# Performance work log

Hardware: AMD Instinct MI355X
Metric: run time of the kernel (lower is better)

Reference implementation:

```python
import jax, jax.numpy as jnp
import numpy as np

ANCHORS = np.array([[10,13],[16,30],[33,23],[30,61],[62,45],[59,119],[116,90],[156,198],[373,326]], dtype=np.float32)
ANCHOR_MASK = [[6,7,8],[3,4,5],[0,1,2]]
CLASS_NUM = 80
IGNORE_THRESH = 0.5


def _bce_mean(z, x):
    # Keras BinaryCrossentropy(from_logits=True) called as a loss object:
    # elementwise sigmoid-CE, mean over last axis, then SUM_OVER_BATCH_SIZE
    # reduction == mean over ALL elements -> scalar.
    ce = jnp.maximum(x, 0.0) - x * z + jnp.log1p(jnp.exp(-jnp.abs(x)))
    return jnp.mean(ce)


def _layer_loss(out, lab, anchors):
    B, gh, gw, _ = out.shape
    A = anchors.shape[0]
    feats = out.reshape(B, gh, gw, A, CLASS_NUM + 5)
    anchors = jnp.asarray(anchors, dtype=jnp.float32)  # [A,2] (w,h)
    inp_wh = jnp.array([gw * 32, gh * 32], dtype=jnp.float32)  # reverse(input_shape)
    grid_wh = jnp.array([gw, gh], dtype=jnp.float32)           # reverse(grid_shape)

    gy, gx = jnp.meshgrid(jnp.arange(gh), jnp.arange(gw), indexing='ij')
    grid = jnp.stack([gx, gy], axis=-1).astype(jnp.float32)[:, :, None, :]  # [gh,gw,1,2]

    pred_xy = (jax.nn.sigmoid(feats[..., 0:2]) + grid) / grid_wh
    pred_wh = jnp.exp(feats[..., 2:4]) * anchors / inp_wh
    pred_box = jnp.concatenate([pred_xy, pred_wh], axis=-1)  # [B,gh,gw,A,4]

    obj = lab[..., 4:5]          # [B,gh,gw,A,1]
    objb = obj != 0.0
    N = gh * gw * A

    def _per_image(args):
        pb, tb, valid = args  # pb: [N,4] predicted, tb: [N,4] label boxes, valid: [N] bool
        b1_xy, b1_wh = pb[:, None, 0:2], pb[:, None, 2:4]
        b2_xy, b2_wh = tb[None, :, 0:2], tb[None, :, 2:4]
        b1_mins, b1_maxes = b1_xy - b1_wh / 2.0, b1_xy + b1_wh / 2.0
        b2_mins, b2_maxes = b2_xy - b2_wh / 2.0, b2_xy + b2_wh / 2.0
        inter_mins = jnp.maximum(b1_mins, b2_mins)
        inter_maxes = jnp.maximum(b1_maxes, b2_maxes)  # faithful to source (uses maximum, not minimum)
        inter_wh = jnp.maximum(inter_maxes - inter_mins, 0.0)
        inter = inter_wh[..., 0] * inter_wh[..., 1]
        a1 = b1_wh[..., 0] * b1_wh[..., 1]
        a2 = b2_wh[..., 0] * b2_wh[..., 1]
        iou = inter / (a1 + a2 - inter)  # [N,N]
        # only true boxes count; empty set -> best=-1 (matches tf reduce_max of empty = -inf)
        iou = jnp.where(valid[None, :], iou, -1.0)
        best_iou = jnp.max(iou, axis=-1)
        return (best_iou < IGNORE_THRESH).astype(jnp.float32)

    ignore = jax.lax.map(_per_image, (pred_box.reshape(B, N, 4),
                                      lab[..., 0:4].reshape(B, N, 4),
                                      objb.reshape(B, N)))
    ignore = jax.lax.stop_gradient(ignore).reshape(B, gh, gw, A, 1)

    raw_true_xy = lab[..., 0:2] * grid_wh - grid
    raw_true_wh = jnp.log(lab[..., 2:4] * inp_wh / anchors)
    raw_true_wh = jnp.where(objb, raw_true_wh, 0.0)
    box_loss_scale = 2.0 - lab[..., 2:3] * lab[..., 3:4]

    bf = jnp.float32(B)
    xy_loss = jnp.sum(obj * box_loss_scale * _bce_mean(raw_true_xy, feats[..., 0:2])) / bf
    wh_loss = jnp.sum(obj * box_loss_scale * 0.5 * jnp.square(raw_true_wh - feats[..., 2:4])) / bf
    conf_bce = _bce_mean(obj, feats[..., 4:5])
    conf_loss = jnp.sum(obj * conf_bce + (1.0 - obj) * conf_bce * ignore) / bf
    class_loss = jnp.sum(obj * _bce_mean(lab[..., 5:], feats[..., 5:])) / bf
    return xy_loss + wh_loss + conf_loss + class_loss


def _make_labels(key, B, g):
    k1, k2, k3, k4 = jax.random.split(key, 4)
    xy = jax.random.uniform(k1, (B, g, g, 3, 2), dtype=jnp.float32)
    wh = jax.random.uniform(k2, (B, g, g, 3, 2), dtype=jnp.float32, minval=0.05, maxval=1.0)
    objness = (jax.random.uniform(k3, (B, g, g, 3, 1)) < 0.02).astype(jnp.float32)
    cls = (jax.random.uniform(k4, (B, g, g, 3, CLASS_NUM)) < 0.05).astype(jnp.float32)
    return jnp.concatenate([xy, wh, objness, cls], axis=-1)


def setup_inputs() -> dict:
    key = jax.random.key(0)
    ks = jax.random.split(key, 6)
    B = 8
    grids = [13, 26, 52]
    out = {}
    for i, g in enumerate(grids):
        out[f'o{i}'] = jax.random.normal(ks[i], (B, g, g, 3 * (CLASS_NUM + 5)), dtype=jnp.float32)
        out[f'l{i}'] = _make_labels(ks[3 + i], B, g)
    return out


def reference(o0, o1, o2, l0, l1, l2):
    outputs = (o0, o1, o2)
    labels = (l0, l1, l2)
    loss = jnp.float32(0.0)
    for l in range(3):
        loss = loss + _layer_loss(outputs[l], labels[l], ANCHORS[ANCHOR_MASK[l]])
    return loss
```

## Files before the change

### kernel.cpp

```cpp
#include <hip/hip_runtime.h>
#include <math.h>

#define BDIM 256
#define NSTREAMB 1769
#define NCELLB 334
#define NBLK_A (NSTREAMB + NCELLB)
#define NB_IGNORE 336
#define SCAP 1024

__device__ __constant__ float c_aw[3][3] = {{116.f,156.f,373.f},{30.f,62.f,59.f},{10.f,16.f,33.f}};
__device__ __constant__ float c_ah[3][3] = {{90.f,198.f,326.f},{61.f,45.f,119.f},{13.f,30.f,23.f}};


__device__ __forceinline__ float bce_fast(float z, float x) {
    float t = __expf(-fabsf(x));
    return fmaxf(x, 0.f) - x * z + __logf(1.f + t);
}
__device__ __forceinline__ float bce4(const float4& z, const float4& x) {
    return bce_fast(z.x, x.x) + bce_fast(z.y, x.y)
         + bce_fast(z.z, x.z) + bce_fast(z.w, x.w);
}

__global__ __launch_bounds__(BDIM) void mega_a(
    const float* __restrict__ o0, const float* __restrict__ l0,
    const float* __restrict__ o1, const float* __restrict__ l1,
    const float* __restrict__ o2, const float* __restrict__ l2,
    double* __restrict__ accq7, int* __restrict__ done,
    double* __restrict__ slotS, double* __restrict__ slotC,
    float4* __restrict__ pbox, float* __restrict__ noobj)
{
    if (blockIdx.x < NSTREAMB) {
        if (blockIdx.x == 0 && threadIdx.x == 0) {
            accq7[0] = 0.0; accq7[1] = 0.0; accq7[2] = 0.0; *done = 0;
        }
        int blk0, n4;
        const float4 *O4, *L4;
        if (blockIdx.x < 85)       { blk0=0;   n4=86190;   O4=(const float4*)o0; L4=(const float4*)l0; }
        else if (blockIdx.x < 422) { blk0=85;  n4=344760;  O4=(const float4*)o1; L4=(const float4*)l1; }
        else                       { blk0=422; n4=1379040; O4=(const float4*)o2; L4=(const float4*)l2; }

        int rb   = (int)blockIdx.x - blk0;
        int base = rb * (BDIM * 4) + (int)threadIdx.x;
        float s0 = 0.f, s1 = 0.f, s2 = 0.f, s3 = 0.f;
        if ((rb + 1) * (BDIM * 4) <= n4) {
            float4 a0 = O4[base];          float4 b0 = L4[base];
            float4 a1 = O4[base +   BDIM]; float4 b1 = L4[base +   BDIM];
            float4 a2 = O4[base + 2*BDIM]; float4 b2 = L4[base + 2*BDIM];
            float4 a3 = O4[base + 3*BDIM]; float4 b3 = L4[base + 3*BDIM];
            s0 = bce4(b0, a0); s1 = bce4(b1, a1);
            s2 = bce4(b2, a2); s3 = bce4(b3, a3);
        } else {
            #pragma unroll
            for (int k = 0; k < 4; k++) {
                int j = base + k * BDIM;
                if (j < n4) { float4 a = O4[j], b = L4[j]; s0 += bce4(b, a); }
            }
        }
        float s = (s0 + s1) + (s2 + s3);
        __shared__ float sb[4];
        #pragma unroll
        for (int off = 32; off > 0; off >>= 1) s += __shfl_down(s, off, 64);
        if ((threadIdx.x & 63) == 0) sb[threadIdx.x >> 6] = s;
        __syncthreads();
        if (threadIdx.x == 0)
            slotS[blockIdx.x] = (double)sb[0] + (double)sb[1]
                              + (double)sb[2] + (double)sb[3];
        return;
    }

    int cb = blockIdx.x - NSTREAMB;
    int layer, cblk0;
    if (cb < 16)      { layer = 0; cblk0 = 0; }
    else if (cb < 80) { layer = 1; cblk0 = 16; }
    else              { layer = 2; cblk0 = 80; }
    const int g     = (layer == 0) ? 13 : (layer == 1) ? 26 : 52;
    const int Nlimg = g * g * 3;
    const int Cl    = 8 * Nlimg;
    const int cbase = (layer == 0) ? 0 : (layer == 1) ? 4056 : 20280;
    const float* O  = (layer == 0) ? o0 : (layer == 1) ? o1 : o2;
    const float* L  = (layer == 0) ? l0 : (layer == 1) ? l1 : l2;
    const float gf  = (float)g;
    const float inp = gf * 32.f;

    int  cell = (cb - cblk0) * BDIM + (int)threadIdx.x;
    bool live = (cell < Cl);
    float s_sub=0.f, s_xy=0.f, s_wh=0.f, s_conf=0.f, s_obj=0.f, s_s1=0.f;
    if (live) {
        const float* op = O + (size_t)cell * 85;
        const float* lp = L + (size_t)cell * 85;
        float x0=op[0], x1=op[1], x2=op[2], x3=op[3], x4=op[4];
        float lx=lp[0], ly=lp[1], lw=lp[2], lh=lp[3], lobj=lp[4];
        int a  = cell % 3;
        int xi = (cell / 3) % g;
        int yi = (cell / (3 * g)) % g;
        float aw = c_aw[layer][a], ah = c_ah[layer][a];

        float c4 = bce_fast(lobj, x4);
        s_sub  = bce_fast(lx,x0) + bce_fast(ly,x1)
               + bce_fast(lw,x2) + bce_fast(lh,x3) + c4;
        s_conf = c4;
        s_obj  = lobj;
        s_xy   = bce_fast(lx*gf - (float)xi, x0) + bce_fast(ly*gf - (float)yi, x1);

        float px = (1.f/(1.f+expf(-x0)) + (float)xi) / gf;
        float py = (1.f/(1.f+expf(-x1)) + (float)yi) / gf;
        float pw = expf(x2) * aw / inp;
        float ph = expf(x3) * ah / inp;
        pbox[cbase + cell]  = make_float4(px, py, pw, ph);
        noobj[cbase + cell] = 1.f - lobj;

        if (lobj != 0.f) {
            float bls = 2.f - lw * lh;
            s_s1 = lobj * bls;
            float dw = logf(lw * inp / aw) - x2;
            float dh = logf(lh * inp / ah) - x3;
            s_wh = lobj * bls * 0.5f * (dw * dw + dh * dh);
        }
    }

    __shared__ float sb6[6][4];
    float v[6] = {s_sub, s_xy, s_wh, s_conf, s_obj, s_s1};
    #pragma unroll
    for (int q = 0; q < 6; q++) {
        float x = v[q];
        #pragma unroll
        for (int off = 32; off > 0; off >>= 1) x += __shfl_down(x, off, 64);
        if ((threadIdx.x & 63) == 0) sb6[q][threadIdx.x >> 6] = x;
    }
    __syncthreads();
    if (threadIdx.x < 6) {
        int q = threadIdx.x;
        slotC[cb * 6 + q] = (double)sb6[q][0] + (double)sb6[q][1]
                          + (double)sb6[q][2] + (double)sb6[q][3];
    }
}

__global__ __launch_bounds__(BDIM) void ignore_fin(
    const float* __restrict__ l0, const float* __restrict__ l1,
    const float* __restrict__ l2,
    double* __restrict__ accq7, int* __restrict__ done,
    const double* __restrict__ slotS, const double* __restrict__ slotC,
    const float4* __restrict__ pbox, const float* __restrict__ noobj,
    float* __restrict__ out)
{
    int layer, img, chunk;
    if (blockIdx.x < 16)      { layer = 0; img = blockIdx.x >> 1; chunk = blockIdx.x & 1; }
    else if (blockIdx.x < 80) { int t = blockIdx.x - 16; layer = 1; img = t >> 3; chunk = t & 7; }
    else                      { int t = blockIdx.x - 80; layer = 2; img = t >> 5; chunk = t & 31; }
    const int g     = (layer == 0) ? 13 : (layer == 1) ? 26 : 52;
    const int Nlimg = g * g * 3;
    const int cbase = (layer == 0) ? 0 : (layer == 1) ? 4056 : 20280;
    const float* L  = (layer == 0) ? l0 : (layer == 1) ? l1 : l2;

    int ci = chunk * BDIM + (int)threadIdx.x;
    bool live = (ci < Nlimg);
    int cell = cbase + img * Nlimg + (live ? ci : 0);

    float pminx=0, pmaxx=0, pminy=0, pmaxy=0, a1=0, nb=0;
    if (live) {
        float4 p = pbox[cell];
        pminx = p.x - p.z*0.5f; pmaxx = p.x + p.z*0.5f;
        pminy = p.y - p.w*0.5f; pmaxy = p.y + p.w*0.5f;
        a1 = p.z * p.w;
        nb = noobj[cell];
    }

    __shared__ int    sIdx[SCAP];
    __shared__ int    sN;
    __shared__ float4 sT[SCAP];
    if (threadIdx.x == 0) sN = 0;
    __syncthreads();
    const float* nob = noobj + cbase + img * Nlimg;
    for (int i = threadIdx.x; i < Nlimg; i += BDIM) {
        if (nob[i] == 0.0f) {
            int p = atomicAdd(&sN, 1);
            if (p < SCAP) sIdx[p] = i;
        }
    }
    __syncthreads();
    int n = min(sN, SCAP);
    for (int i = threadIdx.x; i < n; i += BDIM) {
        const float* lp = L + (size_t)(img * Nlimg + sIdx[i]) * 85;
        sT[i] = make_float4(lp[0], lp[1], lp[2], lp[3]);
    }
    __syncthreads();

    float best = -1.f;
    if (live) {
        for (int j = 0; j < n; j++) {
            float4 t = sT[j];
            float hw = t.z*0.5f, hh = t.w*0.5f;
            float imnx = fmaxf(pminx, t.x - hw);
            float imxx = fmaxf(pmaxx, t.x + hw);
            float imny = fmaxf(pminy, t.y - hh);
            float imxy = fmaxf(pmaxy, t.y + hh);
            float iw = fmaxf(imxx - imnx, 0.f);
            float ih = fmaxf(imxy - imny, 0.f);
            float inter = iw * ih;
            float iou = inter / (a1 + t.z*t.w - inter);
            best = fmaxf(best, iou);
            if (best >= 0.5f) break;
        }
    }

    float v = (live && best < 0.5f) ? nb : 0.f;
    __shared__ float sbr[4];
    #pragma unroll
    for (int off = 32; off > 0; off >>= 1) v += __shfl_down(v, off, 64);
    if ((threadIdx.x & 63) == 0) sbr[threadIdx.x >> 6] = v;
    __syncthreads();
    __shared__ int isLast;
    if (threadIdx.x == 0) {
        double t = (double)sbr[0] + (double)sbr[1] + (double)sbr[2] + (double)sbr[3];
        atomicAdd(&accq7[layer], t);
        __threadfence();
        int old = atomicAdd(done, 1);
        isLast = (old == NB_IGNORE - 1) ? 1 : 0;
    }
    __syncthreads();
    if (!isLast) return;

    __threadfence();
    double qs0=0, qs1=0, qs2=0;
    for (int i = threadIdx.x; i < NSTREAMB; i += BDIM) {
        double x = slotS[i];
        if (i < 85) qs0 += x; else if (i < 422) qs1 += x; else qs2 += x;
    }
    double c00=0,c01=0,c02=0,c03=0,c04=0,c05=0;
    double c10=0,c11=0,c12=0,c13=0,c14=0,c15=0;
    double c20=0,c21=0,c22=0,c23=0,c24=0,c25=0;
#define CSUM(LO, HI, A0,A1,A2,A3,A4,A5)                                      \
    for (int i = (LO)*6 + (int)threadIdx.x; i < (HI)*6; i += BDIM) {         \
        int q = i % 6; double x = slotC[i];                                  \
        if      (q == 0) A0 += x; else if (q == 1) A1 += x;                  \
        else if (q == 2) A2 += x; else if (q == 3) A3 += x;                  \
        else if (q == 4) A4 += x; else             A5 += x;                  \
    }
    CSUM(0,   16,  c00,c01,c02,c03,c04,c05)
    CSUM(16,  80,  c10,c11,c12,c13,c14,c15)
    CSUM(80,  334, c20,c21,c22,c23,c24,c25)

    __shared__ double dsum[21][4];
    {
        double vals[21] = {qs0,qs1,qs2,
                           c00,c01,c02,c03,c04,c05,
                           c10,c11,c12,c13,c14,c15,
                           c20,c21,c22,c23,c24,c25};
        int lane = threadIdx.x & 63, wid = threadIdx.x >> 6;
        #pragma unroll
        for (int k = 0; k < 21; k++) {
            double r = vals[k];
            #pragma unroll
            for (int off = 32; off > 0; off >>= 1) r += __shfl_down(r, off, 64);
            if (lane == 0) dsum[k][wid] = r;
        }
    }
    __syncthreads();
    if (threadIdx.x == 0) {
        double loss = 0.0;
        const int gsz[3] = {13, 26, 52};
        for (int l = 0; l < 3; l++) {
            double C = 8.0 * gsz[l] * gsz[l] * 3.0;
            double Q0 = dsum[l][0] + dsum[l][1] + dsum[l][2] + dsum[l][3];
            double Qs[6];
            for (int j = 0; j < 6; j++) {
                int k = 3 + l * 6 + j;
                Qs[j] = dsum[k][0] + dsum[k][1] + dsum[k][2] + dsum[k][3];
            }
            double q7 = __hip_atomic_load(&accq7[l], __ATOMIC_RELAXED,
                                          __HIP_MEMORY_SCOPE_AGENT);
            double cls = (Q0 - Qs[0]) / (C * 80.0);
            loss += ( (Qs[1]/(C*2.0))*Qs[5] + Qs[2]
                    + (Qs[3]/C)*(Qs[4]+q7) + cls*Qs[4] ) / 8.0;
        }
        out[0] = (float)loss;
    }
}

extern "C" void kernel_launch(void* const* d_in, const int* in_sizes, int n_in,
                              void* d_out, int out_size, void* d_ws, size_t ws_size,
                              hipStream_t stream)
{
    const float* o0 = (const float*)d_in[0];
    const float* l0 = (const float*)d_in[1];
    const float* o1 = (const float*)d_in[2];
    const float* l1 = (const float*)d_in[3];
    const float* o2 = (const float*)d_in[4];
    const float* l2 = (const float*)d_in[5];

    double* accq7 = (double*)d_ws;
    int*    done  = (int*)((char*)d_ws + 24);
    double* slotS = (double*)((char*)d_ws + 64);
    double* slotC = (double*)((char*)d_ws + 14336);
    float4* pbox  = (float4*)((char*)d_ws + 30720);
    float*  noobj = (float*)((char*)d_ws + 1393664);

    mega_a<<<NBLK_A, BDIM, 0, stream>>>(o0, l0, o1, l1, o2, l2,
                                        accq7, done, slotS, slotC, pbox, noobj);
    ignore_fin<<<NB_IGNORE, BDIM, 0, stream>>>(l0, l1, l2,
                                               accq7, done, slotS, slotC,
                                               pbox, noobj, (float*)d_out);
}
```

Measured before the change: 151.9 us.

## Replace atomic last-block finalization with separate finalize kernel; schedule cell blocks first

Drops the atomic accumulation and done-counter last-block pattern from the ignore kernel. Per-block partials now go to a slot array, and a separate single-block kernel reduces them. The mega kernel also reorders its blocks so the cell-processing blocks, which produce pbox and noobj, get dispatched before the streaming BCE blocks. The aim is to remove atomics and fences and finish the dependency-critical work earlier, at the cost of one extra kernel launch.

```diff
diff --git a/kernel.cpp b/kernel.cpp
--- a/kernel.cpp
+++ b/kernel.cpp
@@ -2,9 +2,9 @@
 #include <math.h>
 
 #define BDIM 256
+#define NCELLB 334
 #define NSTREAMB 1769
-#define NCELLB 334
-#define NBLK_A (NSTREAMB + NCELLB)
+#define NBLK_A (NCELLB + NSTREAMB)
 #define NB_IGNORE 336
 #define SCAP 1024
 
@@ -25,21 +25,18 @@
     const float* __restrict__ o0, const float* __restrict__ l0,
     const float* __restrict__ o1, const float* __restrict__ l1,
     const float* __restrict__ o2, const float* __restrict__ l2,
-    double* __restrict__ accq7, int* __restrict__ done,
     double* __restrict__ slotS, double* __restrict__ slotC,
     float4* __restrict__ pbox, float* __restrict__ noobj)
 {
-    if (blockIdx.x < NSTREAMB) {
-        if (blockIdx.x == 0 && threadIdx.x == 0) {
-            accq7[0] = 0.0; accq7[1] = 0.0; accq7[2] = 0.0; *done = 0;
-        }
+    if (blockIdx.x >= NCELLB) {
+        int sb = blockIdx.x - NCELLB;
         int blk0, n4;
         const float4 *O4, *L4;
-        if (blockIdx.x < 85)       { blk0=0;   n4=86190;   O4=(const float4*)o0; L4=(const float4*)l0; }
-        else if (blockIdx.x < 422) { blk0=85;  n4=344760;  O4=(const float4*)o1; L4=(const float4*)l1; }
-        else                       { blk0=422; n4=1379040; O4=(const float4*)o2; L4=(const float4*)l2; }
-
-        int rb   = (int)blockIdx.x - blk0;
+        if (sb < 85)       { blk0=0;   n4=86190;   O4=(const float4*)o0; L4=(const float4*)l0; }
+        else if (sb < 422) { blk0=85;  n4=344760;  O4=(const float4*)o1; L4=(const float4*)l1; }
+        else               { blk0=422; n4=1379040; O4=(const float4*)o2; L4=(const float4*)l2; }
+
+        int rb   = sb - blk0;
         int base = rb * (BDIM * 4) + (int)threadIdx.x;
         float s0 = 0.f, s1 = 0.f, s2 = 0.f, s3 = 0.f;
         if ((rb + 1) * (BDIM * 4) <= n4) {
@@ -57,18 +54,18 @@
             }
         }
         float s = (s0 + s1) + (s2 + s3);
-        __shared__ float sb[4];
+        __shared__ float sb4[4];
         #pragma unroll
         for (int off = 32; off > 0; off >>= 1) s += __shfl_down(s, off, 64);
-        if ((threadIdx.x & 63) == 0) sb[threadIdx.x >> 6] = s;
+        if ((threadIdx.x & 63) == 0) sb4[threadIdx.x >> 6] = s;
         __syncthreads();
         if (threadIdx.x == 0)
-            slotS[blockIdx.x] = (double)sb[0] + (double)sb[1]
-                              + (double)sb[2] + (double)sb[3];
+            slotS[sb] = (double)sb4[0] + (double)sb4[1]
+                      + (double)sb4[2] + (double)sb4[3];
         return;
     }
 
-    int cb = blockIdx.x - NSTREAMB;
+    int cb = blockIdx.x;
     int layer, cblk0;
     if (cb < 16)      { layer = 0; cblk0 = 0; }
     else if (cb < 80) { layer = 1; cblk0 = 16; }
@@ -100,7 +97,8 @@
                + bce_fast(lw,x2) + bce_fast(lh,x3) + c4;
         s_conf = c4;
         s_obj  = lobj;
-        s_xy   = bce_fast(lx*gf - (float)xi, x0) + bce_fast(ly*gf - (float)yi, x1);
+        s_xy   = bce_fast(lx*gf - (float)xi, x0)
+               + bce_fast(ly*gf - (float)yi, x1);
 
         float px = (1.f/(1.f+expf(-x0)) + (float)xi) / gf;
         float py = (1.f/(1.f+expf(-x1)) + (float)yi) / gf;
@@ -135,13 +133,11 @@
     }
 }
 
-__global__ __launch_bounds__(BDIM) void ignore_fin(
+__global__ __launch_bounds__(BDIM) void ignore_nb(
     const float* __restrict__ l0, const float* __restrict__ l1,
     const float* __restrict__ l2,
-    double* __restrict__ accq7, int* __restrict__ done,
-    const double* __restrict__ slotS, const double* __restrict__ slotC,
     const float4* __restrict__ pbox, const float* __restrict__ noobj,
-    float* __restrict__ out)
+    double* __restrict__ slotB)
 {
     int layer, img, chunk;
     if (blockIdx.x < 16)      { layer = 0; img = blockIdx.x >> 1; chunk = blockIdx.x & 1; }
@@ -209,46 +205,42 @@
     for (int off = 32; off > 0; off >>= 1) v += __shfl_down(v, off, 64);
     if ((threadIdx.x & 63) == 0) sbr[threadIdx.x >> 6] = v;
     __syncthreads();
-    __shared__ int isLast;
-    if (threadIdx.x == 0) {
-        double t = (double)sbr[0] + (double)sbr[1] + (double)sbr[2] + (double)sbr[3];
-        atomicAdd(&accq7[layer], t);
-        __threadfence();
-        int old = atomicAdd(done, 1);
-        isLast = (old == NB_IGNORE - 1) ? 1 : 0;
-    }
-    __syncthreads();
-    if (!isLast) return;
-
-    __threadfence();
-    double qs0=0, qs1=0, qs2=0;
+    if (threadIdx.x == 0)
+        slotB[blockIdx.x] = (double)sbr[0] + (double)sbr[1]
+                          + (double)sbr[2] + (double)sbr[3];
+}
+
+__global__ __launch_bounds__(BDIM) void finalize_k(
+    const double* __restrict__ slotS, const double* __restrict__ slotC,
+    const double* __restrict__ slotB, float* __restrict__ out)
+{
+    double vals[24];
+    #pragma unroll
+    for (int k = 0; k < 24; k++) vals[k] = 0.0;
+
     for (int i = threadIdx.x; i < NSTREAMB; i += BDIM) {
         double x = slotS[i];
-        if (i < 85) qs0 += x; else if (i < 422) qs1 += x; else qs2 += x;
-    }
-    double c00=0,c01=0,c02=0,c03=0,c04=0,c05=0;
-    double c10=0,c11=0,c12=0,c13=0,c14=0,c15=0;
-    double c20=0,c21=0,c22=0,c23=0,c24=0,c25=0;
-#define CSUM(LO, HI, A0,A1,A2,A3,A4,A5)                                      \
-    for (int i = (LO)*6 + (int)threadIdx.x; i < (HI)*6; i += BDIM) {         \
-        int q = i % 6; double x = slotC[i];                                  \
-        if      (q == 0) A0 += x; else if (q == 1) A1 += x;                  \
-        else if (q == 2) A2 += x; else if (q == 3) A3 += x;                  \
-        else if (q == 4) A4 += x; else             A5 += x;                  \
-    }
-    CSUM(0,   16,  c00,c01,c02,c03,c04,c05)
-    CSUM(16,  80,  c10,c11,c12,c13,c14,c15)
-    CSUM(80,  334, c20,c21,c22,c23,c24,c25)
-
-    __shared__ double dsum[21][4];
+        int l = (i < 85) ? 0 : (i < 422) ? 1 : 2;
+        vals[l * 8] += x;
+    }
+    for (int i = threadIdx.x; i < NCELLB * 6; i += BDIM) {
+        double x = slotC[i];
+        int q  = i % 6;
+        int cb = i / 6;
+        int l = (cb < 16) ? 0 : (cb < 80) ? 1 : 2;
+        vals[l * 8 + 1 + q] += x;
+    }
+    for (int i = threadIdx.x; i < NB_IGNORE; i += BDIM) {
+        double x = slotB[i];
+        int l = (i < 16) ? 0 : (i < 80) ? 1 : 2;
+        vals[l * 8 + 7] += x;
+    }
+
+    __shared__ double dsum[24][4];
     {
-        double vals[21] = {qs0,qs1,qs2,
-                           c00,c01,c02,c03,c04,c05,
-                           c10,c11,c12,c13,c14,c15,
-                           c20,c21,c22,c23,c24,c25};
         int lane = threadIdx.x & 63, wid = threadIdx.x >> 6;
         #pragma unroll
-        for (int k = 0; k < 21; k++) {
+        for (int k = 0; k < 24; k++) {
             double r = vals[k];
             #pragma unroll
             for (int off = 32; off > 0; off >>= 1) r += __shfl_down(r, off, 64);
@@ -261,17 +253,14 @@
         const int gsz[3] = {13, 26, 52};
         for (int l = 0; l < 3; l++) {
             double C = 8.0 * gsz[l] * gsz[l] * 3.0;
-            double Q0 = dsum[l][0] + dsum[l][1] + dsum[l][2] + dsum[l][3];
-            double Qs[6];
-            for (int j = 0; j < 6; j++) {
-                int k = 3 + l * 6 + j;
-                Qs[j] = dsum[k][0] + dsum[k][1] + dsum[k][2] + dsum[k][3];
-            }
-            double q7 = __hip_atomic_load(&accq7[l], __ATOMIC_RELAXED,
-                                          __HIP_MEMORY_SCOPE_AGENT);
-            double cls = (Q0 - Qs[0]) / (C * 80.0);
-            loss += ( (Qs[1]/(C*2.0))*Qs[5] + Qs[2]
-                    + (Qs[3]/C)*(Qs[4]+q7) + cls*Qs[4] ) / 8.0;
+            double V[8];
+            #pragma unroll
+            for (int k = 0; k < 8; k++)
+                V[k] = dsum[l*8+k][0] + dsum[l*8+k][1]
+                     + dsum[l*8+k][2] + dsum[l*8+k][3];
+            double cls = (V[0] - V[1]) / (C * 80.0);
+            loss += ( (V[2]/(C*2.0))*V[6] + V[3]
+                    + (V[4]/C)*(V[5]+V[7]) + cls*V[5] ) / 8.0;
         }
         out[0] = (float)loss;
     }
@@ -288,16 +277,14 @@
     const float* o2 = (const float*)d_in[4];
     const float* l2 = (const float*)d_in[5];
 
-    double* accq7 = (double*)d_ws;
-    int*    done  = (int*)((char*)d_ws + 24);
     double* slotS = (double*)((char*)d_ws + 64);
     double* slotC = (double*)((char*)d_ws + 14336);
-    float4* pbox  = (float4*)((char*)d_ws + 30720);
-    float*  noobj = (float*)((char*)d_ws + 1393664);
+    double* slotB = (double*)((char*)d_ws + 30720);
+    float4* pbox  = (float4*)((char*)d_ws + 33792);
+    float*  noobj = (float*)((char*)d_ws + 1396608);
 
     mega_a<<<NBLK_A, BDIM, 0, stream>>>(o0, l0, o1, l1, o2, l2,
-                                        accq7, done, slotS, slotC, pbox, noobj);
-    ignore_fin<<<NB_IGNORE, BDIM, 0, stream>>>(l0, l1, l2,
-                                               accq7, done, slotS, slotC,
-                                               pbox, noobj, (float*)d_out);
-}
+                                        slotS, slotC, pbox, noobj);
+    ignore_nb<<<NB_IGNORE, BDIM, 0, stream>>>(l0, l1, l2, pbox, noobj, slotB);
+    finalize_k<<<1, BDIM, 0, stream>>>(slotS, slotC, slotB, (float*)d_out);
+}
```

Result: slower. 160.3 us (+5.6%).
